# Optimization experiments

Measured on AMD Instinct MI355X. Metric: run time of the kernel, lower is better.

## Reference

```python
import jax, jax.numpy as jnp
import numpy as np

N = 8192
IN_F = 128
OUT_F = 128
ALPHA = 0.2  # LeakyReLU negative slope
NEG_INF = -9e15


def setup_inputs() -> dict:
    key = jax.random.key(0)
    k1, k2, k3, k4 = jax.random.split(key, 4)
    h = jax.random.normal(k1, (N, IN_F), dtype=jnp.float32)
    adj = jax.random.randint(k2, (N, N), 0, 2, dtype=jnp.int32)
    # nn.Linear(in, out, bias=False).weight is (out, in); store as (in, out) for h @ W
    W = jax.random.normal(k3, (IN_F, OUT_F), dtype=jnp.float32) * (1.0 / np.sqrt(IN_F))
    # a: (2*out_features, 1), xavier_uniform with gain=1.414
    limit = 1.414 * np.sqrt(6.0 / (2 * OUT_F + 1))
    a = jax.random.uniform(k4, (2 * OUT_F, 1), dtype=jnp.float32, minval=-limit, maxval=limit)
    return {"h": h, "adj": adj, "W": W, "a": a}


def reference(h, adj, W, a):
    Wh = h @ W  # (N, OUT_F)
    a1 = a[:OUT_F, 0]   # score contribution from source node i
    a2 = a[OUT_F:, 0]   # score contribution from target node j
    # e_ij = leakyrelu(Wh_i . a1 + Wh_j . a2) -- avoids the O(N^2 * 2F) concat
    s1 = Wh @ a1  # (N,)
    s2 = Wh @ a2  # (N,)
    e = jax.nn.leaky_relu(s1[:, None] + s2[None, :], negative_slope=ALPHA)  # (N, N)
    masked = jnp.where(adj > 0, e, NEG_INF)
    attention = jax.nn.softmax(masked, axis=1)  # (N, N)
    # dropout is a no-op in eval mode
    h_prime = attention @ Wh  # (N, OUT_F)
    return jax.nn.elu(h_prime)  # concat=True -> ELU
```

## Files before the change

### kernel.cpp

```cpp
#include <hip/hip_runtime.h>
#include <cstdint>
#include <cstddef>


#define NROW 8192
#define FDIM 128

typedef _Float16 f16;
typedef f16 f16x8 __attribute__((ext_vector_type(8)));
typedef float f32x4 __attribute__((ext_vector_type(4)));

#define WS_WHT 0u
#define WS_BP  (2u*1024u*1024u)
#define WS_S12 (4u*1024u*1024u)
#define WS_K12 (WS_S12 + 64u*1024u)
#define WS_EF  (WS_K12 + 64u*1024u)
#define WS_M2  (WS_EF + 64u*1024u)
#define WS_PWS (WS_M2 + 4u*1024u)

__global__ __launch_bounds__(256) void k1_wh(const float* __restrict__ h,
                                             const float* __restrict__ W,
                                             f16* __restrict__ WhT,
                                             f16* __restrict__ Bp,
                                             unsigned* __restrict__ M2key) {
  __shared__ float hT[128 * 36];
  const int t = (int)threadIdx.x;
  const int rb = (int)blockIdx.x * 32;
  if (blockIdx.x == 0 && t == 0) *M2key = 0u;
  const f32x4* hv = (const f32x4*)(h + (size_t)rb * FDIM);
#pragma unroll
  for (int i = 0; i < 4; ++i) {
    int fidx = t + i * 256;
    f32x4 v = hv[fidx];
    int e0 = fidx * 4;
    int r = e0 >> 7, k = e0 & 127;
    hT[(k + 0) * 36 + r] = v[0];
    hT[(k + 1) * 36 + r] = v[1];
    hT[(k + 2) * 36 + r] = v[2];
    hT[(k + 3) * 36 + r] = v[3];
  }
  __syncthreads();
  const int f = t & 127, rh = t >> 7;
  f32x4 z = {0.f, 0.f, 0.f, 0.f};
  f32x4 acc0 = z, acc1 = z, acc2 = z, acc3 = z;
  for (int k = 0; k < 128; ++k) {
    float w = W[k * FDIM + f];
    const f32x4* hp = (const f32x4*)(hT + k * 36 + rh * 16);
    acc0 += hp[0] * w;
    acc1 += hp[1] * w;
    acc2 += hp[2] * w;
    acc3 += hp[3] * w;
  }
  union { f16 hx[16]; uint4 u[2]; } pk;
#pragma unroll
  for (int q = 0; q < 4; ++q) {
    pk.hx[0 + q]  = (f16)acc0[q];
    pk.hx[4 + q]  = (f16)acc1[q];
    pk.hx[8 + q]  = (f16)acc2[q];
    pk.hx[12 + q] = (f16)acc3[q];
  }
  uint4* dst = (uint4*)(WhT + (size_t)f * NROW + rb + rh * 16);
  dst[0] = pk.u[0];
  dst[1] = pk.u[1];
  f16* bdst = Bp + (size_t)blockIdx.x * 4096 + (size_t)(f >> 4) * 512
                 + (size_t)(2 * rh) * 128 + (size_t)(f & 15) * 8;
  *(uint4*)bdst = pk.u[0];
  *(uint4*)(bdst + 128) = pk.u[1];
}

__global__ __launch_bounds__(256) void k1b_s(const f16* __restrict__ WhT,
                                             const float* __restrict__ a,
                                             float2* __restrict__ s12,
                                             unsigned* __restrict__ M2key) {
  __shared__ float part[2][4][64];
  const int l = (int)threadIdx.x & 63;
  const int fc = (int)threadIdx.x >> 6;
  const int r = (int)blockIdx.x * 64 + l;
  float s1 = 0.f, s2 = 0.f;
  for (int f = fc * 32; f < fc * 32 + 32; ++f) {
    float w = (float)WhT[(size_t)f * NROW + r];
    s1 = fmaf(w, a[f], s1);
    s2 = fmaf(w, a[128 + f], s2);
  }
  part[0][fc][l] = s1;
  part[1][fc][l] = s2;
  __syncthreads();
  if (fc == 0) {
    s1 = part[0][0][l] + part[0][1][l] + part[0][2][l] + part[0][3][l];
    s2 = part[1][0][l] + part[1][1][l] + part[1][2][l] + part[1][3][l];
    s12[r] = make_float2(s1, s2);
    float mx = s2;
#pragma unroll
    for (int off = 32; off; off >>= 1) mx = fmaxf(mx, __shfl_xor(mx, off, 64));
    if (l == 0) {
      unsigned key = __float_as_uint(mx);
      key = (key & 0x80000000u) ? ~key : (key | 0x80000000u);
      atomicMax(M2key, key);
    }
  }
}

__global__ __launch_bounds__(256) void k1c_prep(const float2* __restrict__ s12,
                                                const unsigned* __restrict__ M2key,
                                                float2* __restrict__ K12,
                                                f16* __restrict__ Eh,
                                                f16* __restrict__ Fh) {
  int j = (int)blockIdx.x * 256 + (int)threadIdx.x;
  unsigned key = *M2key;
  float M2 = (key & 0x80000000u) ? __uint_as_float(key ^ 0x80000000u)
                                 : __uint_as_float(~key);
  float2 s = s12[j];
  float u = s.x + M2;
  K12[j] = make_float2(__expf(fminf(0.f, 0.8f * u)), __expf(-0.8f * fmaxf(u, 0.f)));
  Eh[j] = (f16)__expf(s.y - M2);
  Fh[j] = (f16)__expf(0.2f * (s.y - M2));
}

__global__ __launch_bounds__(256) void k2_main(const int* __restrict__ adj,
                                               const f16* __restrict__ Bp,
                                               const float2* __restrict__ K12,
                                               const f16* __restrict__ Eh,
                                               const f16* __restrict__ Fh,
                                               float* __restrict__ Pws,
                                               float* __restrict__ Dws,
                                               int jspan) {
  const int tid = (int)threadIdx.x;
  const int L = tid & 63, w = tid >> 6;
  const int wid = (int)blockIdx.x * 4 + w;
  const int rg = wid & 511;
  const int c = wid >> 9;
  const int rb = rg * 16;
  const int m = L & 15, kq = L >> 4;
  const int row = rb + m;
  const int j0 = c * jspan;
  const int niter = jspan >> 5;

  const float2 kk = K12[row];
  f16x8 kap1v, kap2v, bones;
#pragma unroll
  for (int i = 0; i < 8; ++i) {
    kap1v[i] = (f16)kk.x;
    kap2v[i] = (f16)kk.y;
    bones[i] = (f16)1.0f;
  }

  const int* ap = adj + (size_t)row * NROW + j0 + kq * 8;
  const f16* ehp = Eh + j0 + kq * 8;
  const f16* fhp = Fh + j0 + kq * 8;
  const f16* bp = Bp + (size_t)(j0 >> 5) * 4096 + (size_t)L * 8;

  int4 A0s[2], A1s[2];
  f16x8 Er[2], Fr[2];
#pragma unroll
  for (int s = 0; s < 2; ++s) {
    A0s[s] = *(const int4*)(ap + s * 32);
    A1s[s] = *(const int4*)(ap + s * 32 + 4);
    Er[s] = *(const f16x8*)(ehp + s * 32);
    Fr[s] = *(const f16x8*)(fhp + s * 32);
  }

  f32x4 z = {0.f, 0.f, 0.f, 0.f};
  f32x4 acc[8] = {z, z, z, z, z, z, z, z};
  f32x4 accd = z;

  for (int ii = 0; ii < niter; ii += 2) {
#pragma unroll
    for (int s = 0; s < 2; ++s) {
      const int it = ii + s;
      const f16* bt = bp + (size_t)it * 4096;
      f16x8 B0 = *(const f16x8*)(bt);
      f16x8 B1 = *(const f16x8*)(bt + 512);
      f16x8 B2 = *(const f16x8*)(bt + 1024);
      f16x8 B3 = *(const f16x8*)(bt + 1536);
      f16x8 B4 = *(const f16x8*)(bt + 2048);
      f16x8 B5 = *(const f16x8*)(bt + 2560);
      f16x8 B6 = *(const f16x8*)(bt + 3072);
      f16x8 B7 = *(const f16x8*)(bt + 3584);

      f16x8 t = __builtin_elementwise_max(Er[s] * kap1v, Fr[s] * kap2v);
      f16x8 af;
      {
        const int4 a0 = A0s[s], a1 = A1s[s];
        af[0] = (a0.x > 0) ? t[0] : (f16)0.f;
        af[1] = (a0.y > 0) ? t[1] : (f16)0.f;
        af[2] = (a0.z > 0) ? t[2] : (f16)0.f;
        af[3] = (a0.w > 0) ? t[3] : (f16)0.f;
        af[4] = (a1.x > 0) ? t[4] : (f16)0.f;
        af[5] = (a1.y > 0) ? t[5] : (f16)0.f;
        af[6] = (a1.z > 0) ? t[6] : (f16)0.f;
        af[7] = (a1.w > 0) ? t[7] : (f16)0.f;
      }

      const int itn = (it + 2 < niter) ? it + 2 : it;
      Er[s] = *(const f16x8*)(ehp + itn * 32);
      Fr[s] = *(const f16x8*)(fhp + itn * 32);
      A0s[s] = *(const int4*)(ap + itn * 32);
      A1s[s] = *(const int4*)(ap + itn * 32 + 4);

      acc[0] = __builtin_amdgcn_mfma_f32_16x16x32_f16(af, B0, acc[0], 0, 0, 0);
      acc[1] = __builtin_amdgcn_mfma_f32_16x16x32_f16(af, B1, acc[1], 0, 0, 0);
      acc[2] = __builtin_amdgcn_mfma_f32_16x16x32_f16(af, B2, acc[2], 0, 0, 0);
      acc[3] = __builtin_amdgcn_mfma_f32_16x16x32_f16(af, B3, acc[3], 0, 0, 0);
      acc[4] = __builtin_amdgcn_mfma_f32_16x16x32_f16(af, B4, acc[4], 0, 0, 0);
      acc[5] = __builtin_amdgcn_mfma_f32_16x16x32_f16(af, B5, acc[5], 0, 0, 0);
      acc[6] = __builtin_amdgcn_mfma_f32_16x16x32_f16(af, B6, acc[6], 0, 0, 0);
      acc[7] = __builtin_amdgcn_mfma_f32_16x16x32_f16(af, B7, acc[7], 0, 0, 0);
      accd = __builtin_amdgcn_mfma_f32_16x16x32_f16(af, bones, accd, 0, 0, 0);
    }
  }

  if (m == 0) {
#pragma unroll
    for (int reg = 0; reg < 4; ++reg)
      Dws[(size_t)c * NROW + rb + kq * 4 + reg] = accd[reg];
  }

  float* P = Pws + ((size_t)c * NROW + rb) * FDIM + m;
#pragma unroll
  for (int nt = 0; nt < 8; ++nt) {
#pragma unroll
    for (int reg = 0; reg < 4; ++reg) {
      int rr = kq * 4 + reg;
      P[(size_t)rr * FDIM + nt * 16] = acc[nt][reg];
    }
  }
}

__global__ __launch_bounds__(256) void k3_comb(const float* __restrict__ Pws,
                                               const float* __restrict__ Dws,
                                               float* __restrict__ out, int S) {
  int g = (int)blockIdx.x * 256 + (int)threadIdx.x;
  int r = g >> 5, f4 = g & 31;
  f32x4 s = {0.f, 0.f, 0.f, 0.f};
  float den = 0.f;
  for (int c2 = 0; c2 < S; ++c2) {
    s += *(const f32x4*)(Pws + ((size_t)c2 * NROW + r) * FDIM + f4 * 4);
    den += Dws[(size_t)c2 * NROW + r];
  }
  float inv = 1.0f / den;
  f32x4 o;
#pragma unroll
  for (int e = 0; e < 4; ++e) {
    float x = s[e] * inv;
    o[e] = x > 0.f ? x : expm1f(x);
  }
  *(f32x4*)(out + (size_t)r * FDIM + f4 * 4) = o;
}

extern "C" void kernel_launch(void* const* d_in, const int* in_sizes, int n_in,
                              void* d_out, int out_size, void* d_ws, size_t ws_size,
                              hipStream_t stream) {
  const float* h = (const float*)d_in[0];
  const int* adj = (const int*)d_in[1];
  const float* W = (const float*)d_in[2];
  const float* a = (const float*)d_in[3];
  float* out = (float*)d_out;
  char* ws = (char*)d_ws;
  f16* WhT = (f16*)(ws + WS_WHT);
  f16* Bp = (f16*)(ws + WS_BP);
  float2* s12 = (float2*)(ws + WS_S12);
  float2* K12 = (float2*)(ws + WS_K12);
  f16* Eh = (f16*)(ws + WS_EF);
  f16* Fh = (f16*)(ws + WS_EF + 16u * 1024u);
  unsigned* M2 = (unsigned*)(ws + WS_M2);

  const size_t partial_bytes = (size_t)NROW * FDIM * 4;
  int S = (ws_size >= WS_PWS + 8 * partial_bytes + 8 * NROW * 4) ? 8 : 2;
  float* Pws = (float*)(ws + WS_PWS);
  float* Dws = (float*)(ws + WS_PWS + (size_t)S * partial_bytes);
  int jspan = NROW / S;

  k1_wh<<<dim3(256), dim3(256), 0, stream>>>(h, W, WhT, Bp, M2);
  k1b_s<<<dim3(128), dim3(256), 0, stream>>>(WhT, a, s12, M2);
  k1c_prep<<<dim3(32), dim3(256), 0, stream>>>(s12, M2, K12, Eh, Fh);
  k2_main<<<dim3(128 * S), dim3(256), 0, stream>>>(adj, Bp, K12, Eh, Fh, Pws, Dws, jspan);
  k3_comb<<<dim3(1024), dim3(256), 0, stream>>>(Pws, Dws, out, S);
}
```

Before: 470.3 us.

## Stage adjacency tiles through LDS as packed byte masks with coalesced loads

The main kernel now runs one wave per block. For each 1024-column window it first loads a 16-row adjacency tile with fully coalesced 16-byte loads, double-buffered in registers. It packs each group of four int32 values into one 32-bit byte mask and stores it in LDS. The MFMA inner loop then reads an 8-byte mask per step from LDS instead of two int4 global loads per lane. The aim is more bytes in flight and fewer, wider global transactions on the adj stream, which dominates traffic. The cost is extra LDS traffic and an added load phase per window that does not overlap the MFMA loop. The byte-packing assumes adjacency values fit in a byte, which holds for 0/1 inputs.

Result: no change. 466.1 us (-0.9%).

```diff
diff --git a/kernel.cpp b/kernel.cpp
--- a/kernel.cpp
+++ b/kernel.cpp
@@ -116,24 +116,23 @@
   Fh[j] = (f16)__expf(0.2f * (s.y - M2));
 }
 
-__global__ __launch_bounds__(256) void k2_main(const int* __restrict__ adj,
-                                               const f16* __restrict__ Bp,
-                                               const float2* __restrict__ K12,
-                                               const f16* __restrict__ Eh,
-                                               const f16* __restrict__ Fh,
-                                               float* __restrict__ Pws,
-                                               float* __restrict__ Dws,
-                                               int jspan) {
-  const int tid = (int)threadIdx.x;
-  const int L = tid & 63, w = tid >> 6;
-  const int wid = (int)blockIdx.x * 4 + w;
-  const int rg = wid & 511;
-  const int c = wid >> 9;
+__global__ __launch_bounds__(64) void k2_main(const int* __restrict__ adj,
+                                              const f16* __restrict__ Bp,
+                                              const float2* __restrict__ K12,
+                                              const f16* __restrict__ Eh,
+                                              const f16* __restrict__ Fh,
+                                              float* __restrict__ Pws,
+                                              float* __restrict__ Dws,
+                                              int jspan) {
+  __shared__ char mbuf[16 * 1040];
+  const int L = (int)threadIdx.x;
+  const int b = (int)blockIdx.x;
+  const int rg = b & 511;
+  const int c = b >> 9;
   const int rb = rg * 16;
   const int m = L & 15, kq = L >> 4;
   const int row = rb + m;
   const int j0 = c * jspan;
-  const int niter = jspan >> 5;
 
   const float2 kk = K12[row];
   f16x8 kap1v, kap2v, bones;
@@ -144,30 +143,54 @@
     bones[i] = (f16)1.0f;
   }
 
-  const int* ap = adj + (size_t)row * NROW + j0 + kq * 8;
-  const f16* ehp = Eh + j0 + kq * 8;
-  const f16* fhp = Fh + j0 + kq * 8;
-  const f16* bp = Bp + (size_t)(j0 >> 5) * 4096 + (size_t)L * 8;
-
-  int4 A0s[2], A1s[2];
-  f16x8 Er[2], Fr[2];
-#pragma unroll
-  for (int s = 0; s < 2; ++s) {
-    A0s[s] = *(const int4*)(ap + s * 32);
-    A1s[s] = *(const int4*)(ap + s * 32 + 4);
-    Er[s] = *(const f16x8*)(ehp + s * 32);
-    Fr[s] = *(const f16x8*)(fhp + s * 32);
-  }
-
   f32x4 z = {0.f, 0.f, 0.f, 0.f};
   f32x4 acc[8] = {z, z, z, z, z, z, z, z};
   f32x4 accd = z;
 
-  for (int ii = 0; ii < niter; ii += 2) {
-#pragma unroll
-    for (int s = 0; s < 2; ++s) {
-      const int it = ii + s;
-      const f16* bt = bp + (size_t)it * 4096;
+  for (int wb = 0; wb < jspan; wb += 1024) {
+    const int jw = j0 + wb;
+
+    const int* abase = adj + (size_t)rb * NROW + jw;
+    int4 Ra[8], Rb8[8];
+    auto issue = [&](int r, int4* dst) {
+#pragma unroll
+      for (int q = 0; q < 8; ++q) {
+        int rr = 2 * r + (q >> 2), qq = q & 3;
+        dst[q] = *(const int4*)(abase + (size_t)rr * NROW + qq * 256 + L * 4);
+      }
+    };
+    auto packwrite = [&](int r, const int4* src) {
+#pragma unroll
+      for (int q = 0; q < 8; ++q) {
+        int rr = 2 * r + (q >> 2), qq = q & 3;
+        int4 v = src[q];
+        unsigned pb = (unsigned)v.x | ((unsigned)v.y << 8) |
+                      ((unsigned)v.z << 16) | ((unsigned)v.w << 24);
+        *(unsigned*)(mbuf + rr * 1040 + qq * 256 + L * 4) = pb;
+      }
+    };
+    issue(0, Ra);
+    issue(1, Rb8);
+    packwrite(0, Ra); issue(2, Ra);
+    packwrite(1, Rb8); issue(3, Rb8);
+    packwrite(2, Ra); issue(4, Ra);
+    packwrite(3, Rb8); issue(5, Rb8);
+    packwrite(4, Ra); issue(6, Ra);
+    packwrite(5, Rb8); issue(7, Rb8);
+    packwrite(6, Ra);
+    packwrite(7, Rb8);
+
+    const f16* bt0 = Bp + (size_t)(jw >> 5) * 4096 + (size_t)L * 8;
+    const f16* ehp = Eh + jw + kq * 8;
+    const f16* fhp = Fh + jw + kq * 8;
+    const char* mrow = mbuf + m * 1040 + kq * 8;
+
+    f16x8 Ecur = *(const f16x8*)(ehp);
+    f16x8 Fcur = *(const f16x8*)(fhp);
+    uint2 mkc = *(const uint2*)(mrow);
+
+    for (int it = 0; it < 32; ++it) {
+      const f16* bt = bt0 + (size_t)it * 4096;
       f16x8 B0 = *(const f16x8*)(bt);
       f16x8 B1 = *(const f16x8*)(bt + 512);
       f16x8 B2 = *(const f16x8*)(bt + 1024);
@@ -177,25 +200,21 @@
       f16x8 B6 = *(const f16x8*)(bt + 3072);
       f16x8 B7 = *(const f16x8*)(bt + 3584);
 
-      f16x8 t = __builtin_elementwise_max(Er[s] * kap1v, Fr[s] * kap2v);
+      f16x8 t = __builtin_elementwise_max(Ecur * kap1v, Fcur * kap2v);
       f16x8 af;
-      {
-        const int4 a0 = A0s[s], a1 = A1s[s];
-        af[0] = (a0.x > 0) ? t[0] : (f16)0.f;
-        af[1] = (a0.y > 0) ? t[1] : (f16)0.f;
-        af[2] = (a0.z > 0) ? t[2] : (f16)0.f;
-        af[3] = (a0.w > 0) ? t[3] : (f16)0.f;
-        af[4] = (a1.x > 0) ? t[4] : (f16)0.f;
-        af[5] = (a1.y > 0) ? t[5] : (f16)0.f;
-        af[6] = (a1.z > 0) ? t[6] : (f16)0.f;
-        af[7] = (a1.w > 0) ? t[7] : (f16)0.f;
-      }
-
-      const int itn = (it + 2 < niter) ? it + 2 : it;
-      Er[s] = *(const f16x8*)(ehp + itn * 32);
-      Fr[s] = *(const f16x8*)(fhp + itn * 32);
-      A0s[s] = *(const int4*)(ap + itn * 32);
-      A1s[s] = *(const int4*)(ap + itn * 32 + 4);
+      af[0] = (mkc.x & 0x000000FFu) ? t[0] : (f16)0.f;
+      af[1] = (mkc.x & 0x0000FF00u) ? t[1] : (f16)0.f;
+      af[2] = (mkc.x & 0x00FF0000u) ? t[2] : (f16)0.f;
+      af[3] = (mkc.x & 0xFF000000u) ? t[3] : (f16)0.f;
+      af[4] = (mkc.y & 0x000000FFu) ? t[4] : (f16)0.f;
+      af[5] = (mkc.y & 0x0000FF00u) ? t[5] : (f16)0.f;
+      af[6] = (mkc.y & 0x00FF0000u) ? t[6] : (f16)0.f;
+      af[7] = (mkc.y & 0xFF000000u) ? t[7] : (f16)0.f;
+
+      const int itn = (it + 1 < 32) ? it + 1 : it;
+      mkc = *(const uint2*)(mrow + itn * 32);
+      Ecur = *(const f16x8*)(ehp + itn * 32);
+      Fcur = *(const f16x8*)(fhp + itn * 32);
 
       acc[0] = __builtin_amdgcn_mfma_f32_16x16x32_f16(af, B0, acc[0], 0, 0, 0);
       acc[1] = __builtin_amdgcn_mfma_f32_16x16x32_f16(af, B1, acc[1], 0, 0, 0);
@@ -205,7 +224,7 @@
       acc[5] = __builtin_amdgcn_mfma_f32_16x16x32_f16(af, B5, acc[5], 0, 0, 0);
       acc[6] = __builtin_amdgcn_mfma_f32_16x16x32_f16(af, B6, acc[6], 0, 0, 0);
       acc[7] = __builtin_amdgcn_mfma_f32_16x16x32_f16(af, B7, acc[7], 0, 0, 0);
-      accd = __builtin_amdgcn_mfma_f32_16x16x32_f16(af, bones, accd, 0, 0, 0);
+      accd   = __builtin_amdgcn_mfma_f32_16x16x32_f16(af, bones, accd, 0, 0, 0);
     }
   }
 
@@ -273,6 +292,6 @@
   k1_wh<<<dim3(256), dim3(256), 0, stream>>>(h, W, WhT, Bp, M2);
   k1b_s<<<dim3(128), dim3(256), 0, stream>>>(WhT, a, s12, M2);
   k1c_prep<<<dim3(32), dim3(256), 0, stream>>>(s12, M2, K12, Eh, Fh);
-  k2_main<<<dim3(128 * S), dim3(256), 0, stream>>>(adj, Bp, K12, Eh, Fh, Pws, Dws, jspan);
+  k2_main<<<dim3(512 * S), dim3(64), 0, stream>>>(adj, Bp, K12, Eh, Fh, Pws, Dws, jspan);
   k3_comb<<<dim3(1024), dim3(256), 0, stream>>>(Pws, Dws, out, S);
 }
```

## Pack adjacency into bitmask in a pre-pass and feed bits to main kernel

Applied to the files above, without the earlier changes.

Adds a k0_pack kernel that reads the int32 adjacency matrix once and writes a 1-bit-per-edge mask using wavefront ballots. The main MFMA kernel then reads 32-bit mask words instead of int4 adjacency vectors, and the block shape changes from four wavefronts to one wavefront per block. The full 256MB adjacency read still happens in the pack kernel, so the intent is mainly to decouple the streaming read from the MFMA loop. The cost is an extra launch, an 8MB workspace buffer, and a simpler prefetch depth (one iteration instead of two).

Result: faster. 457.8 us (-2.7%).

```diff
diff --git a/kernel.cpp b/kernel.cpp
--- a/kernel.cpp
+++ b/kernel.cpp
@@ -9,6 +9,7 @@
 typedef _Float16 f16;
 typedef f16 f16x8 __attribute__((ext_vector_type(8)));
 typedef float f32x4 __attribute__((ext_vector_type(4)));
+typedef unsigned long long u64;
 
 #define WS_WHT 0u
 #define WS_BP  (2u*1024u*1024u)
@@ -16,7 +17,43 @@
 #define WS_K12 (WS_S12 + 64u*1024u)
 #define WS_EF  (WS_K12 + 64u*1024u)
 #define WS_M2  (WS_EF + 64u*1024u)
-#define WS_PWS (WS_M2 + 4u*1024u)
+#define WS_PM  (WS_M2 + 4u*1024u)
+#define WS_PWS (WS_PM + 8u*1024u*1024u)
+
+__global__ __launch_bounds__(256) void k0_pack(const int* __restrict__ adj,
+                                               u64* __restrict__ pm64) {
+  const int L = (int)threadIdx.x & 63;
+  const int w = (int)threadIdx.x >> 6;
+  const int row = (int)blockIdx.x * 4 + w;
+  const int* ap = adj + (size_t)row * NROW + L;
+  u64* dp = pm64 + (size_t)row * 128;
+  for (int r8 = 0; r8 < 128; r8 += 8) {
+    int v0 = ap[(r8 + 0) * 64];
+    int v1 = ap[(r8 + 1) * 64];
+    int v2 = ap[(r8 + 2) * 64];
+    int v3 = ap[(r8 + 3) * 64];
+    int v4 = ap[(r8 + 4) * 64];
+    int v5 = ap[(r8 + 5) * 64];
+    int v6 = ap[(r8 + 6) * 64];
+    int v7 = ap[(r8 + 7) * 64];
+    u64 b0 = __ballot(v0 > 0);
+    u64 b1 = __ballot(v1 > 0);
+    u64 b2 = __ballot(v2 > 0);
+    u64 b3 = __ballot(v3 > 0);
+    u64 b4 = __ballot(v4 > 0);
+    u64 b5 = __ballot(v5 > 0);
+    u64 b6 = __ballot(v6 > 0);
+    u64 b7 = __ballot(v7 > 0);
+    u64 s01 = (L & 1) ? b1 : b0;
+    u64 s23 = (L & 1) ? b3 : b2;
+    u64 s45 = (L & 1) ? b5 : b4;
+    u64 s67 = (L & 1) ? b7 : b6;
+    u64 s03 = (L & 2) ? s23 : s01;
+    u64 s47 = (L & 2) ? s67 : s45;
+    u64 mv = (L & 4) ? s47 : s03;
+    if (L < 8) dp[r8 + L] = mv;
+  }
+}
 
 __global__ __launch_bounds__(256) void k1_wh(const float* __restrict__ h,
                                              const float* __restrict__ W,
@@ -116,19 +153,18 @@
   Fh[j] = (f16)__expf(0.2f * (s.y - M2));
 }
 
-__global__ __launch_bounds__(256) void k2_main(const int* __restrict__ adj,
-                                               const f16* __restrict__ Bp,
-                                               const float2* __restrict__ K12,
-                                               const f16* __restrict__ Eh,
-                                               const f16* __restrict__ Fh,
-                                               float* __restrict__ Pws,
-                                               float* __restrict__ Dws,
-                                               int jspan) {
-  const int tid = (int)threadIdx.x;
-  const int L = tid & 63, w = tid >> 6;
-  const int wid = (int)blockIdx.x * 4 + w;
-  const int rg = wid & 511;
-  const int c = wid >> 9;
+__global__ __launch_bounds__(64) void k2_main(const unsigned* __restrict__ pm32,
+                                              const f16* __restrict__ Bp,
+                                              const float2* __restrict__ K12,
+                                              const f16* __restrict__ Eh,
+                                              const f16* __restrict__ Fh,
+                                              float* __restrict__ Pws,
+                                              float* __restrict__ Dws,
+                                              int jspan) {
+  const int L = (int)threadIdx.x;
+  const int b = (int)blockIdx.x;
+  const int rg = b & 511;
+  const int c = b >> 9;
   const int rb = rg * 16;
   const int m = L & 15, kq = L >> 4;
   const int row = rb + m;
@@ -144,69 +180,56 @@
     bones[i] = (f16)1.0f;
   }
 
-  const int* ap = adj + (size_t)row * NROW + j0 + kq * 8;
+  const unsigned* pmrow = pm32 + (size_t)row * 256 + (j0 >> 5);
   const f16* ehp = Eh + j0 + kq * 8;
   const f16* fhp = Fh + j0 + kq * 8;
-  const f16* bp = Bp + (size_t)(j0 >> 5) * 4096 + (size_t)L * 8;
-
-  int4 A0s[2], A1s[2];
-  f16x8 Er[2], Fr[2];
-#pragma unroll
-  for (int s = 0; s < 2; ++s) {
-    A0s[s] = *(const int4*)(ap + s * 32);
-    A1s[s] = *(const int4*)(ap + s * 32 + 4);
-    Er[s] = *(const f16x8*)(ehp + s * 32);
-    Fr[s] = *(const f16x8*)(fhp + s * 32);
-  }
+  const f16* bt0 = Bp + (size_t)(j0 >> 5) * 4096 + (size_t)L * 8;
+
+  unsigned mkc = pmrow[0];
+  f16x8 Ecur = *(const f16x8*)(ehp);
+  f16x8 Fcur = *(const f16x8*)(fhp);
 
   f32x4 z = {0.f, 0.f, 0.f, 0.f};
   f32x4 acc[8] = {z, z, z, z, z, z, z, z};
   f32x4 accd = z;
 
-  for (int ii = 0; ii < niter; ii += 2) {
-#pragma unroll
-    for (int s = 0; s < 2; ++s) {
-      const int it = ii + s;
-      const f16* bt = bp + (size_t)it * 4096;
-      f16x8 B0 = *(const f16x8*)(bt);
-      f16x8 B1 = *(const f16x8*)(bt + 512);
-      f16x8 B2 = *(const f16x8*)(bt + 1024);
-      f16x8 B3 = *(const f16x8*)(bt + 1536);
-      f16x8 B4 = *(const f16x8*)(bt + 2048);
-      f16x8 B5 = *(const f16x8*)(bt + 2560);
-      f16x8 B6 = *(const f16x8*)(bt + 3072);
-      f16x8 B7 = *(const f16x8*)(bt + 3584);
-
-      f16x8 t = __builtin_elementwise_max(Er[s] * kap1v, Fr[s] * kap2v);
-      f16x8 af;
-      {
-        const int4 a0 = A0s[s], a1 = A1s[s];
-        af[0] = (a0.x > 0) ? t[0] : (f16)0.f;
-        af[1] = (a0.y > 0) ? t[1] : (f16)0.f;
-        af[2] = (a0.z > 0) ? t[2] : (f16)0.f;
-        af[3] = (a0.w > 0) ? t[3] : (f16)0.f;
-        af[4] = (a1.x > 0) ? t[4] : (f16)0.f;
-        af[5] = (a1.y > 0) ? t[5] : (f16)0.f;
-        af[6] = (a1.z > 0) ? t[6] : (f16)0.f;
-        af[7] = (a1.w > 0) ? t[7] : (f16)0.f;
-      }
-
-      const int itn = (it + 2 < niter) ? it + 2 : it;
-      Er[s] = *(const f16x8*)(ehp + itn * 32);
-      Fr[s] = *(const f16x8*)(fhp + itn * 32);
-      A0s[s] = *(const int4*)(ap + itn * 32);
-      A1s[s] = *(const int4*)(ap + itn * 32 + 4);
-
-      acc[0] = __builtin_amdgcn_mfma_f32_16x16x32_f16(af, B0, acc[0], 0, 0, 0);
-      acc[1] = __builtin_amdgcn_mfma_f32_16x16x32_f16(af, B1, acc[1], 0, 0, 0);
-      acc[2] = __builtin_amdgcn_mfma_f32_16x16x32_f16(af, B2, acc[2], 0, 0, 0);
-      acc[3] = __builtin_amdgcn_mfma_f32_16x16x32_f16(af, B3, acc[3], 0, 0, 0);
-      acc[4] = __builtin_amdgcn_mfma_f32_16x16x32_f16(af, B4, acc[4], 0, 0, 0);
-      acc[5] = __builtin_amdgcn_mfma_f32_16x16x32_f16(af, B5, acc[5], 0, 0, 0);
-      acc[6] = __builtin_amdgcn_mfma_f32_16x16x32_f16(af, B6, acc[6], 0, 0, 0);
-      acc[7] = __builtin_amdgcn_mfma_f32_16x16x32_f16(af, B7, acc[7], 0, 0, 0);
-      accd = __builtin_amdgcn_mfma_f32_16x16x32_f16(af, bones, accd, 0, 0, 0);
-    }
+  for (int it = 0; it < niter; ++it) {
+    const f16* bt = bt0 + (size_t)it * 4096;
+    f16x8 B0 = *(const f16x8*)(bt);
+    f16x8 B1 = *(const f16x8*)(bt + 512);
+    f16x8 B2 = *(const f16x8*)(bt + 1024);
+    f16x8 B3 = *(const f16x8*)(bt + 1536);
+    f16x8 B4 = *(const f16x8*)(bt + 2048);
+    f16x8 B5 = *(const f16x8*)(bt + 2560);
+    f16x8 B6 = *(const f16x8*)(bt + 3072);
+    f16x8 B7 = *(const f16x8*)(bt + 3584);
+
+    f16x8 t = __builtin_elementwise_max(Ecur * kap1v, Fcur * kap2v);
+    const unsigned msh = mkc >> (kq * 8);
+    f16x8 af;
+    af[0] = (msh & 1u)   ? t[0] : (f16)0.f;
+    af[1] = (msh & 2u)   ? t[1] : (f16)0.f;
+    af[2] = (msh & 4u)   ? t[2] : (f16)0.f;
+    af[3] = (msh & 8u)   ? t[3] : (f16)0.f;
+    af[4] = (msh & 16u)  ? t[4] : (f16)0.f;
+    af[5] = (msh & 32u)  ? t[5] : (f16)0.f;
+    af[6] = (msh & 64u)  ? t[6] : (f16)0.f;
+    af[7] = (msh & 128u) ? t[7] : (f16)0.f;
+
+    const int itn = (it + 1 < niter) ? it + 1 : it;
+    mkc = pmrow[itn];
+    Ecur = *(const f16x8*)(ehp + itn * 32);
+    Fcur = *(const f16x8*)(fhp + itn * 32);
+
+    acc[0] = __builtin_amdgcn_mfma_f32_16x16x32_f16(af, B0, acc[0], 0, 0, 0);
+    acc[1] = __builtin_amdgcn_mfma_f32_16x16x32_f16(af, B1, acc[1], 0, 0, 0);
+    acc[2] = __builtin_amdgcn_mfma_f32_16x16x32_f16(af, B2, acc[2], 0, 0, 0);
+    acc[3] = __builtin_amdgcn_mfma_f32_16x16x32_f16(af, B3, acc[3], 0, 0, 0);
+    acc[4] = __builtin_amdgcn_mfma_f32_16x16x32_f16(af, B4, acc[4], 0, 0, 0);
+    acc[5] = __builtin_amdgcn_mfma_f32_16x16x32_f16(af, B5, acc[5], 0, 0, 0);
+    acc[6] = __builtin_amdgcn_mfma_f32_16x16x32_f16(af, B6, acc[6], 0, 0, 0);
+    acc[7] = __builtin_amdgcn_mfma_f32_16x16x32_f16(af, B7, acc[7], 0, 0, 0);
+    accd   = __builtin_amdgcn_mfma_f32_16x16x32_f16(af, bones, accd, 0, 0, 0);
   }
 
   if (m == 0) {
@@ -263,6 +286,7 @@
   f16* Eh = (f16*)(ws + WS_EF);
   f16* Fh = (f16*)(ws + WS_EF + 16u * 1024u);
   unsigned* M2 = (unsigned*)(ws + WS_M2);
+  u64* pm64 = (u64*)(ws + WS_PM);
 
   const size_t partial_bytes = (size_t)NROW * FDIM * 4;
   int S = (ws_size >= WS_PWS + 8 * partial_bytes + 8 * NROW * 4) ? 8 : 2;
@@ -270,9 +294,11 @@
   float* Dws = (float*)(ws + WS_PWS + (size_t)S * partial_bytes);
   int jspan = NROW / S;
 
+  k0_pack<<<dim3(2048), dim3(256), 0, stream>>>(adj, pm64);
   k1_wh<<<dim3(256), dim3(256), 0, stream>>>(h, W, WhT, Bp, M2);
   k1b_s<<<dim3(128), dim3(256), 0, stream>>>(WhT, a, s12, M2);
   k1c_prep<<<dim3(32), dim3(256), 0, stream>>>(s12, M2, K12, Eh, Fh);
-  k2_main<<<dim3(128 * S), dim3(256), 0, stream>>>(adj, Bp, K12, Eh, Fh, Pws, Dws, jspan);
+  k2_main<<<dim3(512 * S), dim3(64), 0, stream>>>((const unsigned*)pm64, Bp, K12, Eh, Fh,
+                                                  Pws, Dws, jspan);
   k3_comb<<<dim3(1024), dim3(256), 0, stream>>>(Pws, Dws, out, S);
 }
```
